# Performance work log

Hardware: AMD Instinct MI355X
Metric: run time of the kernel (lower is better)

## Reference

```python
import jax, jax.numpy as jnp
import numpy as np

V, E, B, T, F, H, WIN, PAD = 50000, 64, 64, 1024, 128, 128, 3, 1


def setup_inputs() -> dict:
    key = jax.random.key(0)
    ks = jax.random.split(key, 14)
    s = 0.05
    ipts = jax.random.randint(ks[0], (B, T), 0, V, dtype=jnp.int32)
    seq_lengths = jax.random.randint(ks[1], (B,), T // 4, T + 1, dtype=jnp.int32)
    hidden = jnp.zeros((2, B, H), jnp.float32)  # (2*nlayers, B, H) bidirectional init state
    emb = (jax.random.normal(ks[2], (V, E), jnp.float32) * s).at[0].set(0.0)  # padding_idx=0
    conv_w = jax.random.normal(ks[3], (F, 1, WIN, E), jnp.float32) * s
    conv_b = jnp.zeros((F,), jnp.float32)
    w_ih_f = jax.random.normal(ks[4], (3 * H, F), jnp.float32) * s
    w_hh_f = jax.random.normal(ks[5], (3 * H, H), jnp.float32) * s
    b_ih_f = jnp.zeros((3 * H,), jnp.float32)
    b_hh_f = jnp.zeros((3 * H,), jnp.float32)
    w_ih_b = jax.random.normal(ks[6], (3 * H, F), jnp.float32) * s
    w_hh_b = jax.random.normal(ks[7], (3 * H, H), jnp.float32) * s
    b_ih_b = jnp.zeros((3 * H,), jnp.float32)
    b_hh_b = jnp.zeros((3 * H,), jnp.float32)
    lin_w = jax.random.normal(ks[8], (1, 2 * H), jnp.float32) * s
    lin_b = jnp.zeros((1,), jnp.float32)
    return dict(ipts=ipts, seq_lengths=seq_lengths, hidden=hidden, emb=emb,
                conv_w=conv_w, conv_b=conv_b,
                w_ih_f=w_ih_f, w_hh_f=w_hh_f, b_ih_f=b_ih_f, b_hh_f=b_hh_f,
                w_ih_b=w_ih_b, w_hh_b=w_hh_b, b_ih_b=b_ih_b, b_hh_b=b_hh_b,
                lin_w=lin_w, lin_b=lin_b)


def _gru(x_tbf, h0, w_ih, w_hh, b_ih, b_hh):
    # PyTorch GRU equations; input gate projections precomputed for all steps.
    xp = jnp.einsum('tbf,gf->tbg', x_tbf, w_ih) + b_ih  # (T,B,3H)

    def step(h, xp_t):
        gh = h @ w_hh.T + b_hh
        xr, xz, xn = jnp.split(xp_t, 3, axis=-1)
        hr, hz, hn = jnp.split(gh, 3, axis=-1)
        r = jax.nn.sigmoid(xr + hr)
        z = jax.nn.sigmoid(xz + hz)
        n = jnp.tanh(xn + r * hn)
        h_new = (1.0 - z) * n + z * h
        return h_new, h_new

    _, out = jax.lax.scan(step, h0, xp)
    return out  # (T,B,H)


def reference(ipts, seq_lengths, hidden, emb, conv_w, conv_b,
              w_ih_f, w_hh_f, b_ih_f, b_hh_f,
              w_ih_b, w_hh_b, b_ih_b, b_hh_b, lin_w, lin_b):
    x = emb[ipts]                                   # (B,T,E)
    c = jax.lax.conv_general_dilated(
        x[:, None, :, :], conv_w, (1, 1), [(PAD, PAD), (0, 0)],
        dimension_numbers=('NCHW', 'OIHW', 'NCHW'))    # (B,F,T,1)
    feats = jnp.transpose(c[..., 0] + conv_b[None, :, None], (0, 2, 1))  # (B,T,F)

    lens = seq_lengths
    t = jnp.arange(T)
    mask = (t[None, :] < lens[:, None]).astype(feats.dtype)             # (B,T)

    # forward direction over padded seq (pad positions masked out of the mean)
    out_f = _gru(jnp.transpose(feats, (1, 0, 2)), hidden[0], w_ih_f, w_hh_f, b_ih_f, b_hh_f)
    # backward direction: packed-sequence semantics -> reverse within the valid length
    rev_idx = jnp.clip(lens[:, None] - 1 - t[None, :], 0, T - 1)        # (B,T)
    feats_rev = jnp.take_along_axis(feats, rev_idx[:, :, None], axis=1)
    out_b = _gru(jnp.transpose(feats_rev, (1, 0, 2)), hidden[1], w_ih_b, w_hh_b, b_ih_b, b_hh_b)

    # masked mean over time (fused segment reduce replacing the python loop)
    m_tb = mask.T[:, :, None]                        # (T,B,1)
    denom = lens.astype(feats.dtype)[:, None]        # (B,1)
    mot_f = (out_f * m_tb).sum(0) / denom            # (B,H)
    mot_b = (out_b * m_tb).sum(0) / denom            # (B,H)
    mot = jnp.concatenate([mot_f, mot_b], axis=-1)   # (B,2H)

    out = jax.nn.sigmoid(mot @ lin_w.T + lin_b)      # (B,1)
    return out.squeeze()
```

## Files before the change

### kernel.cpp

```cpp
#include <hip/hip_runtime.h>


typedef __attribute__((ext_vector_type(8))) unsigned short ushort8;
typedef __attribute__((ext_vector_type(8))) short bf16x8;
typedef __attribute__((ext_vector_type(4))) float f32x4;

__device__ __forceinline__ unsigned short f2bf(float f) {
  unsigned int u = __float_as_uint(f);
  u += 0x7fffu + ((u >> 16) & 1u);
  return (unsigned short)(u >> 16);
}
__device__ __forceinline__ float bf2f(unsigned short us) {
  return __uint_as_float(((unsigned int)us) << 16);
}
#if __has_builtin(__builtin_amdgcn_sdot4)
#define SDOT4(a, b, c) __builtin_amdgcn_sdot4((int)(a), (int)(b), (c), false)
#else
__device__ __forceinline__ int sdot4_sw(int a, int b, int c) {
#pragma unroll
  for (int i = 0; i < 4; ++i)
    c += ((a << (24 - 8 * i)) >> 24) * ((b << (24 - 8 * i)) >> 24);
  return c;
}
#define SDOT4(a, b, c) sdot4_sw((int)(a), (int)(b), (c))
#endif
#define DPP_X1(x) __builtin_amdgcn_update_dpp(0, (x), 0xB1, 0xF, 0xF, true)

__global__ void k0_fuse(const float* __restrict__ conv_w, const float* __restrict__ conv_b,
                        const float* __restrict__ w_ih_f, const float* __restrict__ b_ih_f,
                        const float* __restrict__ w_ih_b, const float* __restrict__ b_ih_b,
                        const float* __restrict__ b_hh_f, const float* __restrict__ b_hh_b,
                        unsigned short* __restrict__ CWb, float* __restrict__ xbias) {
  int flat = blockIdx.x * 256 + threadIdx.x;
  if (flat >= 768 * 192) return;
  int g = flat / 192, k = flat % 192;
  const float* wih = (g < 384) ? w_ih_f : w_ih_b;
  int gg = (g < 384) ? g : g - 384;
  float acc = 0.f;
  for (int f = 0; f < 128; ++f) acc += wih[gg * 128 + f] * conv_w[f * 192 + k];
  CWb[g * 192 + k] = f2bf(acc);
  if (k == 0) {
    const float* bih = (g < 384) ? b_ih_f : b_ih_b;
    const float* bhh = (g < 384) ? b_hh_f : b_hh_b;
    float bb = bih[gg];
    if (gg < 256) bb += bhh[gg];
    for (int f = 0; f < 128; ++f) bb += wih[gg * 128 + f] * conv_b[f];
    xbias[g] = bb;
  }
}

__global__ void k0b_quant(const float* __restrict__ w_hh_f, const float* __restrict__ w_hh_b,
                          unsigned int* __restrict__ Wq8, float* __restrict__ ws) {
  int tid = blockIdx.x * 256 + threadIdx.x;
  int R = tid >> 5, dw = tid & 31;
  if (R >= 768) return;
  int dir = R / 384, rr = R - dir * 384;
  const float* w = (dir ? w_hh_b : w_hh_f) + (size_t)rr * 128 + dw * 4;
  float4 v = *reinterpret_cast<const float4*>(w);
  float am = fmaxf(fmaxf(fabsf(v.x), fabsf(v.y)), fmaxf(fabsf(v.z), fabsf(v.w)));
#pragma unroll
  for (int m = 1; m < 32; m <<= 1) am = fmaxf(am, __shfl_xor(am, m));
  float inv = (am > 0.f) ? 127.f / am : 0.f;
  int q0 = (int)rintf(v.x * inv), q1 = (int)rintf(v.y * inv);
  int q2 = (int)rintf(v.z * inv), q3 = (int)rintf(v.w * inv);
  unsigned int pk = (q0 & 255) | ((q1 & 255) << 8) | ((q2 & 255) << 16) | ((q3 & 255) << 24);
  Wq8[R * 32 + dw] = pk;
  if (dw == 0) ws[R] = am / 16129.f;
}

__global__ __launch_bounds__(256) void k1_gemm(const int* __restrict__ ipts,
                                               const float* __restrict__ emb,
                                               const unsigned short* __restrict__ CWb,
                                               const float* __restrict__ xbias,
                                               unsigned short* __restrict__ xp) {
  __shared__ __align__(16) unsigned short xs[130][72];
  __shared__ __align__(16) unsigned short wsb[128][200];
  const int bid = blockIdx.x;
  const int gb = bid % 6, tb = bid / 6;
  const int b = tb >> 3, t0 = (tb & 7) << 7, g0 = gb << 7;
  const int tid = threadIdx.x;

  for (int c = tid; c < 130 * 16; c += 256) {
    int row = c >> 4, cc = c & 15;
    int t = t0 - 1 + row;
    float4 v = make_float4(0.f, 0.f, 0.f, 0.f);
    if (t >= 0 && t < 1024) {
      int tok = ipts[b * 1024 + t];
      v = *reinterpret_cast<const float4*>(emb + (size_t)tok * 64 + cc * 4);
    }
    ushort4 pv;
    pv.x = f2bf(v.x); pv.y = f2bf(v.y); pv.z = f2bf(v.z); pv.w = f2bf(v.w);
    *reinterpret_cast<ushort4*>(&xs[row][cc * 4]) = pv;
  }
  for (int c = tid; c < 128 * 24; c += 256) {
    int g = c / 24, cc = c % 24;
    *reinterpret_cast<ushort8*>(&wsb[g][cc * 8]) =
        *reinterpret_cast<const ushort8*>(CWb + (size_t)(g0 + g) * 192 + cc * 8);
  }
  __syncthreads();

  const int lane = tid & 63, wid = tid >> 6;
  const int wy = wid >> 1, wx = wid & 1;
  const int ln15 = lane & 15, lhi = lane >> 4;

  f32x4 acc[4][4];
#pragma unroll
  for (int i = 0; i < 4; ++i)
#pragma unroll
    for (int j = 0; j < 4; ++j) acc[i][j] = (f32x4){0.f, 0.f, 0.f, 0.f};

#pragma unroll
  for (int kk = 0; kk < 6; ++kk) {
    const int w = kk >> 1;
    const int e0 = (kk & 1) * 32 + lhi * 8;
    const int k0 = kk * 32 + lhi * 8;
    bf16x8 a[4], bb[4];
#pragma unroll
    for (int i = 0; i < 4; ++i)
      a[i] = *reinterpret_cast<const bf16x8*>(&xs[wy * 64 + i * 16 + ln15 + w][e0]);
#pragma unroll
    for (int j = 0; j < 4; ++j)
      bb[j] = *reinterpret_cast<const bf16x8*>(&wsb[wx * 64 + j * 16 + ln15][k0]);
#pragma unroll
    for (int i = 0; i < 4; ++i)
#pragma unroll
      for (int j = 0; j < 4; ++j)
        acc[i][j] = __builtin_amdgcn_mfma_f32_16x16x32_bf16(a[i], bb[j], acc[i][j], 0, 0, 0);
  }

  float bias[4];
#pragma unroll
  for (int j = 0; j < 4; ++j) bias[j] = xbias[g0 + wx * 64 + j * 16 + ln15];

  unsigned short* outp = xp + (size_t)(b * 1024 + t0 + wy * 64) * 768 + g0 + wx * 64;
#pragma unroll
  for (int i = 0; i < 4; ++i)
#pragma unroll
    for (int r = 0; r < 4; ++r) {
      int m = i * 16 + lhi * 4 + r;
#pragma unroll
      for (int j = 0; j < 4; ++j)
        outp[(size_t)m * 768 + j * 16 + ln15] = f2bf(acc[i][j][r] + bias[j]);
    }
}

__global__ __launch_bounds__(256, 1) void k2_scan(
    const int* __restrict__ seqlen, const float* __restrict__ hidden,
    const float* __restrict__ b_hh_f, const float* __restrict__ b_hh_b,
    const unsigned int* __restrict__ Wq8, const float* __restrict__ ws,
    const unsigned short* __restrict__ xp, float* __restrict__ mot) {
  __shared__ __align__(16) unsigned int hq[2][32];
  const int tid = threadIdx.x;
  const int b = blockIdx.x & 63, dir = blockIdx.x >> 6;
  const int row = tid >> 1;
  const int half = tid & 1;
  const float* bhh = dir ? b_hh_b : b_hh_f;

  uint4 Wq[3][4];
#pragma unroll
  for (int g = 0; g < 3; ++g) {
    const uint4* rp = reinterpret_cast<const uint4*>(
        Wq8 + (size_t)(dir * 384 + g * 128 + row) * 32 + half * 16);
#pragma unroll
    for (int c = 0; c < 4; ++c)
      asm volatile("global_load_dwordx4 %0, %1, off"
                   : "=v"(Wq[g][c]) : "v"(rp + c) : "memory");
  }
  asm volatile("s_waitcnt vmcnt(0)" ::: "memory");
  __builtin_amdgcn_sched_barrier(0);

  const float sc0 = ws[dir * 384 + row];
  const float sc1 = ws[dir * 384 + 128 + row];
  const float sc2 = ws[dir * 384 + 256 + row];
  const float bh2 = bhh[256 + row];

  const int len = seqlen[b];
  float h = hidden[(size_t)(dir * 64 + b) * 128 + row];
  float acc = 0.f;
  if (!half) {
    int q = (int)rintf(h * 127.f) & 255;
    reinterpret_cast<unsigned char*>(&hq[0][0])[row] = (unsigned char)q;
  }

  const unsigned short* xpb = xp + (size_t)b * (1024 * 768) + dir * 384 + row;
  unsigned int xa0, xa1, xa2, xb0, xb1, xb2;
  int row2;
  {
    const int r0 = dir ? (len - 1) : 0;
    const int r1 = dir ? (len - 2) : 1;
    const unsigned short* q0 = xpb + (size_t)r0 * 768;
    const unsigned short* q1 = xpb + (size_t)r1 * 768;
    asm volatile("global_load_ushort %0, %1, off"            : "=v"(xa0) : "v"(q0) : "memory");
    asm volatile("global_load_ushort %0, %1, off offset:256" : "=v"(xa1) : "v"(q0) : "memory");
    asm volatile("global_load_ushort %0, %1, off offset:512" : "=v"(xa2) : "v"(q0) : "memory");
    asm volatile("global_load_ushort %0, %1, off"            : "=v"(xb0) : "v"(q1) : "memory");
    asm volatile("global_load_ushort %0, %1, off offset:256" : "=v"(xb1) : "v"(q1) : "memory");
    asm volatile("global_load_ushort %0, %1, off offset:512" : "=v"(xb2) : "v"(q1) : "memory");
    row2 = dir ? (len - 3 >= 0 ? len - 3 : 0) : (2 < len ? 2 : len - 1);
  }
  asm volatile("s_waitcnt lgkmcnt(0)" ::: "memory");
  __builtin_amdgcn_s_barrier();
  __builtin_amdgcn_sched_barrier(0);

#define K2_STEP(T_, CUR_, X0_, X1_, X2_)                                              \
  {                                                                                   \
    asm volatile("s_waitcnt vmcnt(3)" ::: "memory");                                  \
    __builtin_amdgcn_sched_barrier(0);                                                \
    const float xr = bf2f((unsigned short)(X0_));                                     \
    const float xz = bf2f((unsigned short)(X1_));                                     \
    const float xn = bf2f((unsigned short)(X2_));                                     \
    {                                                                                 \
      const unsigned short* pp = xpb + (size_t)row2 * 768;                            \
      asm volatile("global_load_ushort %0, %1, off"            : "=v"(X0_) : "v"(pp) : "memory"); \
      asm volatile("global_load_ushort %0, %1, off offset:256" : "=v"(X1_) : "v"(pp) : "memory"); \
      asm volatile("global_load_ushort %0, %1, off offset:512" : "=v"(X2_) : "v"(pp) : "memory"); \
      row2 = dir ? (row2 > 0 ? row2 - 1 : 0) : (row2 + 1 < len ? row2 + 1 : len - 1); \
    }                                                                                 \
    int ar = 0, az = 0, an = 0;                                                       \
    _Pragma("unroll")                                                                 \
    for (int c = 0; c < 4; ++c) {                                                     \
      const uint4 hv = *reinterpret_cast<const uint4*>(&hq[CUR_][half * 16 + c * 4]); \
      ar = SDOT4(Wq[0][c].x, hv.x, ar); ar = SDOT4(Wq[0][c].y, hv.y, ar);             \
      ar = SDOT4(Wq[0][c].z, hv.z, ar); ar = SDOT4(Wq[0][c].w, hv.w, ar);             \
      az = SDOT4(Wq[1][c].x, hv.x, az); az = SDOT4(Wq[1][c].y, hv.y, az);             \
      az = SDOT4(Wq[1][c].z, hv.z, az); az = SDOT4(Wq[1][c].w, hv.w, az);             \
      an = SDOT4(Wq[2][c].x, hv.x, an); an = SDOT4(Wq[2][c].y, hv.y, an);             \
      an = SDOT4(Wq[2][c].z, hv.z, an); an = SDOT4(Wq[2][c].w, hv.w, an);             \
    }                                                                                 \
    ar += DPP_X1(ar); az += DPP_X1(az); an += DPP_X1(an);                             \
    const float rr = 1.f / (1.f + __expf(-(xr + sc0 * (float)ar)));                   \
    const float zz = 1.f / (1.f + __expf(-(xz + sc1 * (float)az)));                   \
    const float na = xn + rr * (sc2 * (float)an + bh2);                               \
    const float e2 = __expf(2.f * na);                                                \
    const float nn = (e2 - 1.f) / (e2 + 1.f);                                         \
    const float hnew = (1.f - zz) * nn + zz * h;                                      \
    if ((T_) < len) {                                                                 \
      h = hnew; acc += hnew;                                                          \
      if (!half) {                                                                    \
        int q = (int)rintf(hnew * 127.f) & 255;                                       \
        reinterpret_cast<unsigned char*>(&hq[(CUR_) ^ 1][0])[row] = (unsigned char)q; \
      }                                                                               \
    }                                                                                 \
    asm volatile("s_waitcnt lgkmcnt(0)" ::: "memory");                                \
    __builtin_amdgcn_s_barrier();                                                     \
    __builtin_amdgcn_sched_barrier(0);                                                \
  }

  const int len2 = (len + 1) & ~1;
  for (int t = 0; t < len2; t += 2) {
    K2_STEP(t, 0, xa0, xa1, xa2);
    K2_STEP(t + 1, 1, xb0, xb1, xb2);
  }
#undef K2_STEP

  if (!half) mot[(size_t)b * 256 + dir * 128 + row] = acc / (float)len;
}

__global__ void k3_final(const float* __restrict__ mot, const float* __restrict__ lin_w,
                         const float* __restrict__ lin_b, float* __restrict__ out) {
  int tid = threadIdx.x;
  int b = tid >> 2, part = tid & 3;
  float s = 0.f;
  for (int i = 0; i < 64; ++i) s += mot[b * 256 + part * 64 + i] * lin_w[part * 64 + i];
  s += __shfl_xor(s, 1);
  s += __shfl_xor(s, 2);
  if (part == 0) out[b] = 1.f / (1.f + __expf(-(s + lin_b[0])));
}

extern "C" void kernel_launch(void* const* d_in, const int* in_sizes, int n_in,
                              void* d_out, int out_size, void* d_ws, size_t ws_size,
                              hipStream_t stream) {
  const int*   ipts    = (const int*)d_in[0];
  const int*   seqlen  = (const int*)d_in[1];
  const float* hidden  = (const float*)d_in[2];
  const float* emb     = (const float*)d_in[3];
  const float* conv_w  = (const float*)d_in[4];
  const float* conv_b  = (const float*)d_in[5];
  const float* w_ih_f  = (const float*)d_in[6];
  const float* w_hh_f  = (const float*)d_in[7];
  const float* b_ih_f  = (const float*)d_in[8];
  const float* b_hh_f  = (const float*)d_in[9];
  const float* w_ih_b  = (const float*)d_in[10];
  const float* w_hh_b  = (const float*)d_in[11];
  const float* b_ih_b  = (const float*)d_in[12];
  const float* b_hh_b  = (const float*)d_in[13];
  const float* lin_w   = (const float*)d_in[14];
  const float* lin_b   = (const float*)d_in[15];

  char* ws_ = (char*)d_ws;
  unsigned short* CWb = (unsigned short*)(ws_);
  float* xbias = (float*)(ws_ + 294912);
  float* mot   = (float*)(ws_ + 298240);
  unsigned int* Wq8 = (unsigned int*)(ws_ + 363776);
  float* wsc   = (float*)(ws_ + 462080);
  unsigned short* xp = (unsigned short*)(ws_ + 1048576);
  float* out = (float*)d_out;

  hipLaunchKernelGGL(k0_fuse, dim3(576), dim3(256), 0, stream,
                     conv_w, conv_b, w_ih_f, b_ih_f, w_ih_b, b_ih_b, b_hh_f, b_hh_b,
                     CWb, xbias);
  hipLaunchKernelGGL(k0b_quant, dim3(96), dim3(256), 0, stream,
                     w_hh_f, w_hh_b, Wq8, wsc);
  hipLaunchKernelGGL(k1_gemm, dim3(3072), dim3(256), 0, stream,
                     ipts, emb, CWb, xbias, xp);
  hipLaunchKernelGGL(k2_scan, dim3(128), dim3(256), 0, stream,
                     seqlen, hidden, b_hh_f, b_hh_b, Wq8, wsc, xp, mot);
  hipLaunchKernelGGL(k3_final, dim3(1), dim3(256), 0, stream, mot, lin_w, lin_b, out);
}
```

Baseline: 483.4 us.

## Compute two hidden rows per thread in GRU scan, halving block size

Each thread of the recurrent scan kernel now handles two hidden units instead of one. The block shrinks from 256 to 128 threads, going from four wavefronts to two. The aim is to make the per-step barrier cheaper and to use dword loads for the input projections. In exchange each thread does twice the SDOT4 work and holds twice the weight registers on the serial critical path. The step update is also rewritten with fmaf.

```diff
diff --git a/kernel.cpp b/kernel.cpp
--- a/kernel.cpp
+++ b/kernel.cpp
@@ -144,7 +144,7 @@
     }
 }
 
-__global__ __launch_bounds__(256, 1) void k2_scan(
+__global__ __launch_bounds__(128, 1) void k2_scan(
     const int* __restrict__ seqlen, const float* __restrict__ hidden,
     const float* __restrict__ b_hh_f, const float* __restrict__ b_hh_b,
     const unsigned int* __restrict__ Wq8, const float* __restrict__ ws,
@@ -152,50 +152,56 @@
   __shared__ __align__(16) unsigned int hq[2][32];
   const int tid = threadIdx.x;
   const int b = blockIdx.x & 63, dir = blockIdx.x >> 6;
-  const int row = tid >> 1;
-  const int half = tid & 1;
+  const int q = tid >> 1;
+  const int kh = tid & 1;
   const float* bhh = dir ? b_hh_b : b_hh_f;
 
-  uint4 Wq[3][4];
-#pragma unroll
-  for (int g = 0; g < 3; ++g) {
-    const uint4* rp = reinterpret_cast<const uint4*>(
-        Wq8 + (size_t)(dir * 384 + g * 128 + row) * 32 + half * 16);
-#pragma unroll
-    for (int c = 0; c < 4; ++c)
-      asm volatile("global_load_dwordx4 %0, %1, off"
-                   : "=v"(Wq[g][c]) : "v"(rp + c) : "memory");
-  }
+  uint4 Wq[3][2][4];
+#pragma unroll
+  for (int g = 0; g < 3; ++g)
+#pragma unroll
+    for (int rr = 0; rr < 2; ++rr) {
+      const uint4* rp = reinterpret_cast<const uint4*>(
+          Wq8 + (size_t)(dir * 384 + g * 128 + 2 * q + rr) * 32 + kh * 16);
+#pragma unroll
+      for (int c = 0; c < 4; ++c)
+        asm volatile("global_load_dwordx4 %0, %1, off"
+                     : "=v"(Wq[g][rr][c]) : "v"(rp + c) : "memory");
+    }
   asm volatile("s_waitcnt vmcnt(0)" ::: "memory");
   __builtin_amdgcn_sched_barrier(0);
 
-  const float sc0 = ws[dir * 384 + row];
-  const float sc1 = ws[dir * 384 + 128 + row];
-  const float sc2 = ws[dir * 384 + 256 + row];
-  const float bh2 = bhh[256 + row];
+  float sc[3][2], bh2[2];
+#pragma unroll
+  for (int g = 0; g < 3; ++g)
+#pragma unroll
+    for (int rr = 0; rr < 2; ++rr) sc[g][rr] = ws[dir * 384 + g * 128 + 2 * q + rr];
+  bh2[0] = bhh[256 + 2 * q];
+  bh2[1] = bhh[256 + 2 * q + 1];
 
   const int len = seqlen[b];
-  float h = hidden[(size_t)(dir * 64 + b) * 128 + row];
-  float acc = 0.f;
-  if (!half) {
-    int q = (int)rintf(h * 127.f) & 255;
-    reinterpret_cast<unsigned char*>(&hq[0][0])[row] = (unsigned char)q;
-  }
-
-  const unsigned short* xpb = xp + (size_t)b * (1024 * 768) + dir * 384 + row;
+  float h0 = hidden[(size_t)(dir * 64 + b) * 128 + 2 * q];
+  float h1 = hidden[(size_t)(dir * 64 + b) * 128 + 2 * q + 1];
+  float acc0 = 0.f, acc1 = 0.f;
+  if (!kh) {
+    int q0 = (int)rintf(h0 * 127.f) & 255, q1 = (int)rintf(h1 * 127.f) & 255;
+    reinterpret_cast<unsigned short*>(&hq[0][0])[q] = (unsigned short)(q0 | (q1 << 8));
+  }
+
+  const unsigned short* xpb = xp + (size_t)b * (1024 * 768) + dir * 384 + 2 * q;
   unsigned int xa0, xa1, xa2, xb0, xb1, xb2;
   int row2;
   {
     const int r0 = dir ? (len - 1) : 0;
     const int r1 = dir ? (len - 2) : 1;
-    const unsigned short* q0 = xpb + (size_t)r0 * 768;
-    const unsigned short* q1 = xpb + (size_t)r1 * 768;
-    asm volatile("global_load_ushort %0, %1, off"            : "=v"(xa0) : "v"(q0) : "memory");
-    asm volatile("global_load_ushort %0, %1, off offset:256" : "=v"(xa1) : "v"(q0) : "memory");
-    asm volatile("global_load_ushort %0, %1, off offset:512" : "=v"(xa2) : "v"(q0) : "memory");
-    asm volatile("global_load_ushort %0, %1, off"            : "=v"(xb0) : "v"(q1) : "memory");
-    asm volatile("global_load_ushort %0, %1, off offset:256" : "=v"(xb1) : "v"(q1) : "memory");
-    asm volatile("global_load_ushort %0, %1, off offset:512" : "=v"(xb2) : "v"(q1) : "memory");
+    const unsigned short* p0 = xpb + (size_t)r0 * 768;
+    const unsigned short* p1 = xpb + (size_t)r1 * 768;
+    asm volatile("global_load_dword %0, %1, off"            : "=v"(xa0) : "v"(p0) : "memory");
+    asm volatile("global_load_dword %0, %1, off offset:256" : "=v"(xa1) : "v"(p0) : "memory");
+    asm volatile("global_load_dword %0, %1, off offset:512" : "=v"(xa2) : "v"(p0) : "memory");
+    asm volatile("global_load_dword %0, %1, off"            : "=v"(xb0) : "v"(p1) : "memory");
+    asm volatile("global_load_dword %0, %1, off offset:256" : "=v"(xb1) : "v"(p1) : "memory");
+    asm volatile("global_load_dword %0, %1, off offset:512" : "=v"(xb2) : "v"(p1) : "memory");
     row2 = dir ? (len - 3 >= 0 ? len - 3 : 0) : (2 < len ? 2 : len - 1);
   }
   asm volatile("s_waitcnt lgkmcnt(0)" ::: "memory");
@@ -206,39 +212,52 @@
   {                                                                                   \
     asm volatile("s_waitcnt vmcnt(3)" ::: "memory");                                  \
     __builtin_amdgcn_sched_barrier(0);                                                \
-    const float xr = bf2f((unsigned short)(X0_));                                     \
-    const float xz = bf2f((unsigned short)(X1_));                                     \
-    const float xn = bf2f((unsigned short)(X2_));                                     \
+    const float xr0 = bf2f((unsigned short)(X0_)), xr1 = bf2f((unsigned short)((X0_) >> 16)); \
+    const float xz0 = bf2f((unsigned short)(X1_)), xz1 = bf2f((unsigned short)((X1_) >> 16)); \
+    const float xn0 = bf2f((unsigned short)(X2_)), xn1 = bf2f((unsigned short)((X2_) >> 16)); \
     {                                                                                 \
       const unsigned short* pp = xpb + (size_t)row2 * 768;                            \
-      asm volatile("global_load_ushort %0, %1, off"            : "=v"(X0_) : "v"(pp) : "memory"); \
-      asm volatile("global_load_ushort %0, %1, off offset:256" : "=v"(X1_) : "v"(pp) : "memory"); \
-      asm volatile("global_load_ushort %0, %1, off offset:512" : "=v"(X2_) : "v"(pp) : "memory"); \
+      asm volatile("global_load_dword %0, %1, off"            : "=v"(X0_) : "v"(pp) : "memory"); \
+      asm volatile("global_load_dword %0, %1, off offset:256" : "=v"(X1_) : "v"(pp) : "memory"); \
+      asm volatile("global_load_dword %0, %1, off offset:512" : "=v"(X2_) : "v"(pp) : "memory"); \
       row2 = dir ? (row2 > 0 ? row2 - 1 : 0) : (row2 + 1 < len ? row2 + 1 : len - 1); \
     }                                                                                 \
-    int ar = 0, az = 0, an = 0;                                                       \
+    int r0s = 0, z0s = 0, n0s = 0, r1s = 0, z1s = 0, n1s = 0;                         \
     _Pragma("unroll")                                                                 \
     for (int c = 0; c < 4; ++c) {                                                     \
-      const uint4 hv = *reinterpret_cast<const uint4*>(&hq[CUR_][half * 16 + c * 4]); \
-      ar = SDOT4(Wq[0][c].x, hv.x, ar); ar = SDOT4(Wq[0][c].y, hv.y, ar);             \
-      ar = SDOT4(Wq[0][c].z, hv.z, ar); ar = SDOT4(Wq[0][c].w, hv.w, ar);             \
-      az = SDOT4(Wq[1][c].x, hv.x, az); az = SDOT4(Wq[1][c].y, hv.y, az);             \
-      az = SDOT4(Wq[1][c].z, hv.z, az); az = SDOT4(Wq[1][c].w, hv.w, az);             \
-      an = SDOT4(Wq[2][c].x, hv.x, an); an = SDOT4(Wq[2][c].y, hv.y, an);             \
-      an = SDOT4(Wq[2][c].z, hv.z, an); an = SDOT4(Wq[2][c].w, hv.w, an);             \
+      const uint4 hv = *reinterpret_cast<const uint4*>(&hq[CUR_][kh * 16 + c * 4]);   \
+      r0s = SDOT4(Wq[0][0][c].x, hv.x, r0s); r0s = SDOT4(Wq[0][0][c].y, hv.y, r0s);   \
+      r0s = SDOT4(Wq[0][0][c].z, hv.z, r0s); r0s = SDOT4(Wq[0][0][c].w, hv.w, r0s);   \
+      r1s = SDOT4(Wq[0][1][c].x, hv.x, r1s); r1s = SDOT4(Wq[0][1][c].y, hv.y, r1s);   \
+      r1s = SDOT4(Wq[0][1][c].z, hv.z, r1s); r1s = SDOT4(Wq[0][1][c].w, hv.w, r1s);   \
+      z0s = SDOT4(Wq[1][0][c].x, hv.x, z0s); z0s = SDOT4(Wq[1][0][c].y, hv.y, z0s);   \
+      z0s = SDOT4(Wq[1][0][c].z, hv.z, z0s); z0s = SDOT4(Wq[1][0][c].w, hv.w, z0s);   \
+      z1s = SDOT4(Wq[1][1][c].x, hv.x, z1s); z1s = SDOT4(Wq[1][1][c].y, hv.y, z1s);   \
+      z1s = SDOT4(Wq[1][1][c].z, hv.z, z1s); z1s = SDOT4(Wq[1][1][c].w, hv.w, z1s);   \
+      n0s = SDOT4(Wq[2][0][c].x, hv.x, n0s); n0s = SDOT4(Wq[2][0][c].y, hv.y, n0s);   \
+      n0s = SDOT4(Wq[2][0][c].z, hv.z, n0s); n0s = SDOT4(Wq[2][0][c].w, hv.w, n0s);   \
+      n1s = SDOT4(Wq[2][1][c].x, hv.x, n1s); n1s = SDOT4(Wq[2][1][c].y, hv.y, n1s);   \
+      n1s = SDOT4(Wq[2][1][c].z, hv.z, n1s); n1s = SDOT4(Wq[2][1][c].w, hv.w, n1s);   \
     }                                                                                 \
-    ar += DPP_X1(ar); az += DPP_X1(az); an += DPP_X1(an);                             \
-    const float rr = 1.f / (1.f + __expf(-(xr + sc0 * (float)ar)));                   \
-    const float zz = 1.f / (1.f + __expf(-(xz + sc1 * (float)az)));                   \
-    const float na = xn + rr * (sc2 * (float)an + bh2);                               \
-    const float e2 = __expf(2.f * na);                                                \
-    const float nn = (e2 - 1.f) / (e2 + 1.f);                                         \
-    const float hnew = (1.f - zz) * nn + zz * h;                                      \
+    r0s += DPP_X1(r0s); z0s += DPP_X1(z0s); n0s += DPP_X1(n0s);                       \
+    r1s += DPP_X1(r1s); z1s += DPP_X1(z1s); n1s += DPP_X1(n1s);                       \
+          \
+    const float rr0 = 1.f / (1.f + __expf(-fmaf(sc[0][0], (float)r0s, xr0)));         \
+    const float rr1 = 1.f / (1.f + __expf(-fmaf(sc[0][1], (float)r1s, xr1)));         \
+    const float zz0 = 1.f / (1.f + __expf(-fmaf(sc[1][0], (float)z0s, xz0)));         \
+    const float zz1 = 1.f / (1.f + __expf(-fmaf(sc[1][1], (float)z1s, xz1)));         \
+    const float na0 = fmaf(rr0, fmaf(sc[2][0], (float)n0s, bh2[0]), xn0);             \
+    const float na1 = fmaf(rr1, fmaf(sc[2][1], (float)n1s, bh2[1]), xn1);             \
+    const float e20 = __expf(2.f * na0), e21 = __expf(2.f * na1);                     \
+    const float nn0 = (e20 - 1.f) / (e20 + 1.f), nn1 = (e21 - 1.f) / (e21 + 1.f);     \
+    const float hn0 = fmaf(zz0, h0 - nn0, nn0);                                       \
+    const float hn1 = fmaf(zz1, h1 - nn1, nn1);                                       \
     if ((T_) < len) {                                                                 \
-      h = hnew; acc += hnew;                                                          \
-      if (!half) {                                                                    \
-        int q = (int)rintf(hnew * 127.f) & 255;                                       \
-        reinterpret_cast<unsigned char*>(&hq[(CUR_) ^ 1][0])[row] = (unsigned char)q; \
+      h0 = hn0; h1 = hn1; acc0 += hn0; acc1 += hn1;                                   \
+      if (!kh) {                                                                      \
+        int q0 = (int)rintf(hn0 * 127.f) & 255, q1 = (int)rintf(hn1 * 127.f) & 255;   \
+        reinterpret_cast<unsigned short*>(&hq[(CUR_) ^ 1][0])[q] =                    \
+            (unsigned short)(q0 | (q1 << 8));                                         \
       }                                                                               \
     }                                                                                 \
     asm volatile("s_waitcnt lgkmcnt(0)" ::: "memory");                                \
@@ -253,7 +272,11 @@
   }
 #undef K2_STEP
 
-  if (!half) mot[(size_t)b * 256 + dir * 128 + row] = acc / (float)len;
+  if (!kh) {
+    const float inv = 1.f / (float)len;
+    *reinterpret_cast<float2*>(&mot[(size_t)b * 256 + dir * 128 + 2 * q]) =
+        make_float2(acc0 * inv, acc1 * inv);
+  }
 }
 
 __global__ void k3_final(const float* __restrict__ mot, const float* __restrict__ lin_w,
@@ -303,7 +326,7 @@
                      w_hh_f, w_hh_b, Wq8, wsc);
   hipLaunchKernelGGL(k1_gemm, dim3(3072), dim3(256), 0, stream,
                      ipts, emb, CWb, xbias, xp);
-  hipLaunchKernelGGL(k2_scan, dim3(128), dim3(256), 0, stream,
+  hipLaunchKernelGGL(k2_scan, dim3(128), dim3(128), 0, stream,
                      seqlen, hidden, b_hh_f, b_hh_b, Wq8, wsc, xp, mot);
   hipLaunchKernelGGL(k3_final, dim3(1), dim3(256), 0, stream, mot, lin_w, lin_b, out);
 }
```

Result: slower. 647.1 us (+33.9%).
